# Kernel optimization log

Measured on AMD Instinct MI355X. Metric: run time of the kernel, lower is better.

Reference implementation:

```python
import jax, jax.numpy as jnp
import numpy as np

H, DST, DCONV, EXP = 640, 16, 4, 2
DIN = H * EXP          # 1280
DTR = -(-H // 16)      # 40
EPS = 1e-6


def rmsnorm(x, w):
    rms = jnp.sqrt(jnp.mean(x * x, axis=-1, keepdims=True) + EPS)
    return x / rms * w


def bitlinear(x, w, nw):
    # RMSNorm -> ternary weight quant + int8 activation quant (STE)
    x = rmsnorm(x, nw)
    alpha = jnp.maximum(jnp.mean(jnp.abs(w)), 1e-10)
    wq = jnp.clip(jnp.round(w / alpha), -1.0, 1.0)
    wq = w + jax.lax.stop_gradient(wq - w)
    gamma = jnp.maximum(jnp.max(jnp.abs(x), axis=-1, keepdims=True), 1e-10)
    xq = jnp.clip(jnp.round(x * 127.0 / gamma), -128.0, 127.0)
    xq = x + jax.lax.stop_gradient(xq - x)
    return (xq @ wq.T) * (alpha * gamma / 127.0)


def causal_conv1d(x, cw, cb):
    # x: [B,L,D]; depthwise causal conv, kernel DCONV
    pad = DCONV - 1
    xp = jnp.pad(x, ((0, 0), (pad, 0), (0, 0)))
    L = x.shape[1]
    out = jnp.zeros_like(x)
    for k in range(DCONV):
        out = out + xp[:, pad - k:pad - k + L, :] * cw[:, k]
    return out + cb


def selective_scan(x, dt, B_mat, C_mat, A_log):
    # x,dt: [B,L,D]; B_mat,C_mat: [B,L,N]; A_log: [D,N]
    A = -jnp.exp(A_log)
    dA = jnp.exp(A[None, None] * dt[..., None])                 # [B,L,D,N]
    dBx = dt[..., None] * B_mat[:, :, None, :] * x[..., None]   # [B,L,D,N]
    dA_t = jnp.moveaxis(dA, 1, 0)
    dBx_t = jnp.moveaxis(dBx, 1, 0)
    C_t = jnp.moveaxis(C_mat, 1, 0)

    def step(h, inp):
        da, dbx, c = inp
        h = da * h + dbx
        y = jnp.sum(h * c[:, None, :], axis=-1)  # [B,D]
        return h, y

    h0 = jnp.zeros(x.shape[:1] + (x.shape[2], A_log.shape[1]), x.dtype)
    _, ys = jax.lax.scan(step, h0, (dA_t, dBx_t, C_t))
    return jnp.moveaxis(ys, 0, 1)  # [B,L,D]


def setup_inputs() -> dict:
    key = jax.random.key(0)
    ks = jax.random.split(key, 10)
    sc_in = 1.0 / np.sqrt(H)
    sc_din = 1.0 / np.sqrt(DIN)
    A = np.tile(np.arange(1, DST + 1, dtype=np.float32)[None, :], (DIN, 1))
    return {
        "x": jax.random.normal(ks[0], (2, 2048, H), jnp.float32),
        "norm_w": jnp.ones((H,), jnp.float32),
        "in_w": jax.random.normal(ks[1], (DIN * 2, H), jnp.float32) * sc_in,
        "in_nw": jnp.ones((H,), jnp.float32),
        "conv_w": jax.random.normal(ks[2], (DIN, DCONV), jnp.float32) * 0.1,
        "conv_b": jnp.zeros((DIN,), jnp.float32),
        "dtu_w": jax.random.normal(ks[3], (DTR, DIN), jnp.float32) * sc_din,
        "dtu_nw": jnp.ones((DIN,), jnp.float32),
        "dtd_w": jax.random.normal(ks[4], (DIN, DTR), jnp.float32) / np.sqrt(DTR),
        "dtd_b": jnp.zeros((DIN,), jnp.float32),
        "Bp_w": jax.random.normal(ks[5], (DST, DIN), jnp.float32) * sc_din,
        "Bp_nw": jnp.ones((DIN,), jnp.float32),
        "Cp_w": jax.random.normal(ks[6], (DST, DIN), jnp.float32) * sc_din,
        "Cp_nw": jnp.ones((DIN,), jnp.float32),
        "A_log": jnp.asarray(np.log(A)),
        "D": jnp.ones((DIN,), jnp.float32),
        "out_w": jax.random.normal(ks[7], (H, DIN), jnp.float32) * sc_din,
        "out_nw": jnp.ones((DIN,), jnp.float32),
    }


def reference(x, norm_w, in_w, in_nw, conv_w, conv_b, dtu_w, dtu_nw, dtd_w, dtd_b,
              Bp_w, Bp_nw, Cp_w, Cp_nw, A_log, D, out_w, out_nw):
    residual = x
    xn = rmsnorm(x, norm_w)
    xz = bitlinear(xn, in_w, in_nw)
    x_path, z = jnp.split(xz, 2, axis=-1)
    x_path = causal_conv1d(x_path, conv_w, conv_b)
    x_path = jax.nn.silu(x_path)
    dt = jax.nn.softplus(bitlinear(x_path, dtu_w, dtu_nw) @ dtd_w.T + dtd_b)
    B_mat = bitlinear(x_path, Bp_w, Bp_nw)
    C_mat = bitlinear(x_path, Cp_w, Cp_nw)
    y = selective_scan(x_path, dt, B_mat, C_mat, A_log)
    y = y + x_path * D
    y = y * jax.nn.silu(z)
    return bitlinear(y, out_w, out_nw) + residual
```

## Files before the change

### kernel.cpp

```cpp
#include <hip/hip_runtime.h>
#include <hip/hip_bf16.h>
#include <cmath>

#define NROWS 4096
#define H_    640
#define DIN_  1280
#define DXZ   2560
#define DTR_  40
#define DST_  16
#define LSEQ  2048
#define EPS_  1e-6f
#define NCH   64
#define CL    32
#define NDG   20
#define KSPLIT 8
#define KCH (DIN_ / KSPLIT)
#define LOG2E 1.4426950408889634f
#define RLOG2E 0.6931471805599453f

typedef __attribute__((ext_vector_type(8))) short short8;
typedef __attribute__((ext_vector_type(4))) float f32x4;
typedef unsigned short ushort_t;

__device__ __forceinline__ float bf2f(short u) {
    return __uint_as_float((unsigned)(unsigned short)u << 16);
}
__device__ __forceinline__ short f2bfs(float x) { return (short)(__float_as_uint(x) >> 16); }

#define GLD16(gp, lp) __builtin_amdgcn_global_load_lds( \
    (const __attribute__((address_space(1))) unsigned int*)(unsigned long long)(gp), \
    (__attribute__((address_space(3))) unsigned int*)(unsigned int)(unsigned long long)(lp), 16, 0, 0)

__device__ __forceinline__ float wave_sum64(float v) {
    v += __shfl_xor(v, 1);  v += __shfl_xor(v, 2);  v += __shfl_xor(v, 4);
    v += __shfl_xor(v, 8);  v += __shfl_xor(v, 16); v += __shfl_xor(v, 32);
    return v;
}
__device__ __forceinline__ float wave_max64(float v) {
    v = fmaxf(v, __shfl_xor(v, 1));  v = fmaxf(v, __shfl_xor(v, 2));
    v = fmaxf(v, __shfl_xor(v, 4));  v = fmaxf(v, __shfl_xor(v, 8));
    v = fmaxf(v, __shfl_xor(v, 16)); v = fmaxf(v, __shfl_xor(v, 32));
    return v;
}
__device__ __forceinline__ float block_sum4(float v, float* red4) {
    v = wave_sum64(v);
    if ((threadIdx.x & 63) == 0) red4[threadIdx.x >> 6] = v;
    __syncthreads();
    return (red4[0] + red4[1]) + (red4[2] + red4[3]);
}
__device__ __forceinline__ float block_max4(float v, float* red4) {
    v = wave_max64(v);
    if ((threadIdx.x & 63) == 0) red4[threadIdx.x >> 6] = v;
    __syncthreads();
    return fmaxf(fmaxf(red4[0], red4[1]), fmaxf(red4[2], red4[3]));
}
__device__ __forceinline__ float block_reduce_sum256(float v, float* red) {
    int tid = threadIdx.x;
    red[tid] = v; __syncthreads();
    for (int o = 128; o; o >>= 1) { if (tid < o) red[tid] += red[tid + o]; __syncthreads(); }
    float r = red[0]; __syncthreads();
    return r;
}

__global__ __launch_bounds__(256) void k_pre(const float* __restrict__ x,
                                             const float* __restrict__ norm_w,
                                             const float* __restrict__ in_nw,
                                             const float* __restrict__ w0, const float* __restrict__ w1,
                                             const float* __restrict__ w2, const float* __restrict__ w3,
                                             const float* __restrict__ w4,
                                             int n0, int n1, int n2, int n3, int n4,
                                             __hip_bfloat16* __restrict__ xq, float* __restrict__ gamma,
                                             float* __restrict__ partials) {
    __shared__ float red[256];
    const int tid = threadIdx.x;
    if (blockIdx.x < NROWS) {
        const int r = blockIdx.x;
        const float* xr = x + (size_t)r * H_;
        const bool has2 = (tid < H_ - 512);
        float v0 = xr[tid], v1 = xr[tid + 256], v2 = has2 ? xr[tid + 512] : 0.f;
        float sum = block_sum4(v0 * v0 + v1 * v1 + v2 * v2, red);
        float r1 = 1.f / sqrtf(sum / H_ + EPS_);
        v0 *= r1 * norm_w[tid];
        v1 *= r1 * norm_w[tid + 256];
        if (has2) v2 *= r1 * norm_w[tid + 512];
        sum = block_sum4(v0 * v0 + v1 * v1 + v2 * v2, red + 4);
        float r2 = 1.f / sqrtf(sum / H_ + EPS_);
        v0 *= r2 * in_nw[tid];
        v1 *= r2 * in_nw[tid + 256];
        if (has2) v2 *= r2 * in_nw[tid + 512];
        float mx = fmaxf(fmaxf(fabsf(v0), fabsf(v1)), fabsf(v2));
        float g = fmaxf(block_max4(mx, red + 8), 1e-10f);
        if (tid == 0) gamma[r] = g;
        float s = 127.f / g;
        __hip_bfloat16* o = xq + (size_t)r * H_;
        o[tid]       = __float2bfloat16(fminf(fmaxf(rintf(v0 * s), -128.f), 127.f));
        o[tid + 256] = __float2bfloat16(fminf(fmaxf(rintf(v1 * s), -128.f), 127.f));
        if (has2) o[tid + 512] = __float2bfloat16(fminf(fmaxf(rintf(v2 * s), -128.f), 127.f));
    } else {
        const int flat = blockIdx.x - NROWS;
        const int wi = flat >> 8, xb = flat & 255;
        const float* w = (wi == 0) ? w0 : (wi == 1) ? w1 : (wi == 2) ? w2 : (wi == 3) ? w3 : w4;
        const int n = (wi == 0) ? n0 : (wi == 1) ? n1 : (wi == 2) ? n2 : (wi == 3) ? n3 : n4;
        float s = 0.f;
        for (int i = xb * 256 + tid; i < n; i += 65536) s += fabsf(w[i]);
        float t = block_reduce_sum256(s, red);
        if (tid == 0) partials[wi * 256 + xb] = t;
    }
}

__global__ __launch_bounds__(256) void absmean_final5(const float* __restrict__ partials,
                                                      int n0, int n1, int n2, int n3, int n4,
                                                      float* __restrict__ alphas) {
    const int wi = blockIdx.x;
    const int n = (wi == 0) ? n0 : (wi == 1) ? n1 : (wi == 2) ? n2 : (wi == 3) ? n3 : n4;
    __shared__ double red[256];
    double s = (double)partials[wi * 256 + threadIdx.x];
    red[threadIdx.x] = s; __syncthreads();
    for (int o = 128; o; o >>= 1) { if (threadIdx.x < o) red[threadIdx.x] += red[threadIdx.x + o]; __syncthreads(); }
    if (threadIdx.x == 0) alphas[wi] = fmaxf((float)(red[0] / (double)n), 1e-10f);
}

__global__ __launch_bounds__(256) void k_quant_build(const float* __restrict__ in_w,
                                                     const float* __restrict__ out_w,
                                                     const float* __restrict__ dtu_w,
                                                     const float* __restrict__ Bp_w,
                                                     const float* __restrict__ Cp_w,
                                                     const float* __restrict__ alphas,
                                                     __hip_bfloat16* __restrict__ q_in,
                                                     __hip_bfloat16* __restrict__ q_out,
                                                     ushort_t* __restrict__ wq_sk) {
    const int tid = threadIdx.x;
    if (blockIdx.x < 6400) {
        int i = blockIdx.x * 256 + tid;
        float a = alphas[0];
        ((ushort_t*)q_in)[i] = (ushort_t)f2bfs(fminf(fmaxf(rintf(in_w[i] / a), -1.f), 1.f));
    } else if (blockIdx.x < 9600) {
        int i = (blockIdx.x - 6400) * 256 + tid;
        float a = alphas[4];
        ((ushort_t*)q_out)[i] = (ushort_t)f2bfs(fminf(fmaxf(rintf(out_w[i] / a), -1.f), 1.f));
    } else {
        int idx = (blockIdx.x - 9600) * 256 + tid;
        int t = idx / 2560, rem = idx % 2560, kb = rem / 64, l = rem % 64;
        int nloc = l & 15, kg = l >> 4;
        float alpha; const float* src; int row; bool valid = true;
        if (t < 3)      { alpha = alphas[1]; src = dtu_w; row = t * 16 + nloc; valid = (row < 40); }
        else if (t == 3){ alpha = alphas[2]; src = Bp_w;  row = nloc; }
        else            { alpha = alphas[3]; src = Cp_w;  row = nloc; }
        int k0 = kb * 32 + kg * 8;
        short8 outv;
#pragma unroll
        for (int e = 0; e < 8; ++e) {
            float q = valid ? fminf(fmaxf(rintf(src[(size_t)row * DIN_ + k0 + e] / alpha), -1.f), 1.f) : 0.f;
            outv[e] = f2bfs(q);
        }
        *(short8*)(wq_sk + (size_t)idx * 8) = outv;
    }
}

template<int BM, int BN>
__global__ __launch_bounds__(256) void k_gemm_mfma(const ushort_t* __restrict__ Aq,
                                                   const ushort_t* __restrict__ Wq,
                                                   const float* __restrict__ alpha_p,
                                                   const float* __restrict__ gamma,
                                                   const float* __restrict__ residual,
                                                   float* __restrict__ out,
                                                   int M, int N, int K) {
    constexpr int FM = BM / 32, FN = BN / 32;
    constexpr int NL = (BM + BN) / 64;
    __shared__ ushort_t As[2][BM * 32];
    __shared__ ushort_t Bs[2][BN * 32];
    const int tid = threadIdx.x;
    const int w = tid >> 6, lane = tid & 63;
    const int wm = w >> 1, wn = w & 1;
    const int nwg = gridDim.x * gridDim.y;
    const int hw = blockIdx.y * gridDim.x + blockIdx.x;
    const int work = (nwg % 8 == 0) ? ((hw & 7) * (nwg >> 3) + (hw >> 3)) : hw;
    const int row0 = (work / gridDim.x) * BM;
    const int col0 = (work % gridDim.x) * BN;
    f32x4 acc[FM][FN] = {};

    auto stage = [&](int buf, int k0) {
        #pragma unroll
        for (int q = 0; q < BM / 64; ++q) {
            int c = w * BM + q * 64 + lane;
            int row = c >> 2;
            int uslot = (c & 3) ^ (row & 3);
            GLD16(Aq + (size_t)(row0 + row) * K + k0 + uslot * 8,
                  (char*)As[buf] + (w * BM + q * 64) * 16);
        }
        #pragma unroll
        for (int q = 0; q < BN / 64; ++q) {
            int c = w * BN + q * 64 + lane;
            int row = c >> 2;
            int uslot = (c & 3) ^ (row & 3);
            GLD16(Wq + (size_t)(col0 + row) * K + k0 + uslot * 8,
                  (char*)Bs[buf] + (w * BN + q * 64) * 16);
        }
    };

    stage(0, 0);
    const int NT = K >> 5;
    for (int t = 0; t < NT; ++t) {
        const int cur = t & 1;
        if (t + 1 < NT) {
            stage(cur ^ 1, (t + 1) << 5);
            if constexpr (NL == 2)      asm volatile("s_waitcnt vmcnt(2)" ::: "memory");
            else if constexpr (NL == 3) asm volatile("s_waitcnt vmcnt(3)" ::: "memory");
            else                        asm volatile("s_waitcnt vmcnt(4)" ::: "memory");
        } else {
            asm volatile("s_waitcnt vmcnt(0)" ::: "memory");
        }
        __builtin_amdgcn_s_barrier();

        short8 a[FM], b[FN];
        #pragma unroll
        for (int i = 0; i < FM; ++i) {
            int row = wm * (BM / 2) + i * 16 + (lane & 15);
            int byt = row * 64 + (((lane >> 4) ^ (row & 3)) << 4);
            a[i] = *(const short8*)((const char*)As[cur] + byt);
        }
        #pragma unroll
        for (int j = 0; j < FN; ++j) {
            int row = wn * (BN / 2) + j * 16 + (lane & 15);
            int byt = row * 64 + (((lane >> 4) ^ (row & 3)) << 4);
            b[j] = *(const short8*)((const char*)Bs[cur] + byt);
        }
        #pragma unroll
        for (int i = 0; i < FM; ++i)
            #pragma unroll
            for (int j = 0; j < FN; ++j)
                acc[i][j] = __builtin_amdgcn_mfma_f32_16x16x32_bf16(a[i], b[j], acc[i][j], 0, 0, 0);
        asm volatile("" ::: "memory");
        __builtin_amdgcn_s_barrier();
    }

    const float alpha = alpha_p[0];
    #pragma unroll
    for (int i = 0; i < FM; ++i) {
        #pragma unroll
        for (int r = 0; r < 4; ++r) {
            int row = row0 + wm * (BM / 2) + i * 16 + (lane >> 4) * 4 + r;
            float s = alpha * gamma[row] * (1.f / 127.f);
            #pragma unroll
            for (int j = 0; j < FN; ++j) {
                int col = col0 + wn * (BN / 2) + j * 16 + (lane & 15);
                float o = acc[i][j][r] * s;
                if (residual) o += residual[(size_t)row * N + col];
                out[(size_t)row * N + col] = o;
            }
        }
    }
}

__global__ __launch_bounds__(256) void k_conv_norm(const float* __restrict__ xz,
                                                   const float* __restrict__ cw, const float* __restrict__ cb,
                                                   const float* __restrict__ dtu_nw,
                                                   const float* __restrict__ Bp_nw,
                                                   const float* __restrict__ Cp_nw,
                                                   float* __restrict__ xp,
                                                   float* __restrict__ rinv_out, float* __restrict__ g3) {
    const int row = blockIdx.x, tid = threadIdx.x;
    const int l = row & (LSEQ - 1);
    __shared__ float red4[16];
    float vv[5];
    float ss = 0.f;
#pragma unroll
    for (int j = 0; j < 5; ++j) {
        int d = tid + j * 256;
        f32x4 c4 = *(const f32x4*)(cw + (size_t)d * 4);
        const float* base = xz + (size_t)row * DXZ + d;
        float s = cb[d] + base[0] * c4[0];
        if (l >= 1) s += base[-(ptrdiff_t)DXZ] * c4[1];
        if (l >= 2) s += base[-(ptrdiff_t)(2 * DXZ)] * c4[2];
        if (l >= 3) s += base[-(ptrdiff_t)(3 * DXZ)] * c4[3];
        float v = s / (1.f + __builtin_amdgcn_exp2f(-s * LOG2E));
        vv[j] = v;
        ss += v * v;
        xp[(size_t)row * DIN_ + d] = v;
    }
    float sum = block_sum4(ss, red4);
    float rms = 1.f / sqrtf(sum / DIN_ + EPS_);
    float m0 = 0.f, m1 = 0.f, m2 = 0.f;
#pragma unroll
    for (int j = 0; j < 5; ++j) {
        int d = tid + j * 256;
        float t = vv[j] * rms;
        m0 = fmaxf(m0, fabsf(t * dtu_nw[d]));
        m1 = fmaxf(m1, fabsf(t * Bp_nw[d]));
        m2 = fmaxf(m2, fabsf(t * Cp_nw[d]));
    }
    float g0 = block_max4(m0, red4 + 4);
    float g1 = block_max4(m1, red4 + 8);
    float g2 = block_max4(m2, red4 + 12);
    if (tid == 0) {
        rinv_out[row]       = rms;
        g3[row]             = fmaxf(g0, 1e-10f);
        g3[NROWS + row]     = fmaxf(g1, 1e-10f);
        g3[2 * NROWS + row] = fmaxf(g2, 1e-10f);
    }
}

__global__ __launch_bounds__(256) void k_skinny_mfma(const float* __restrict__ xp,
                                                     const float* __restrict__ rinv,
                                                     const float* __restrict__ dtu_nw,
                                                     const float* __restrict__ Bp_nw,
                                                     const float* __restrict__ Cp_nw,
                                                     const float* __restrict__ g3,
                                                     const ushort_t* __restrict__ wq_sk,
                                                     float* __restrict__ dtu_acc,
                                                     float* __restrict__ B_acc,
                                                     float* __restrict__ C_acc) {
    const int tid = threadIdx.x;
    const int w = tid >> 6, l = tid & 63;
    const int row0 = blockIdx.x * 64;
    const int kc0 = blockIdx.y * KCH;
    __shared__ float s_xp[64 * 36];
    __shared__ float s_nw[3 * KCH];
    for (int i = tid; i < 3 * KCH; i += 256) {
        int m = i / KCH, j = i - m * KCH;
        const float* nw = (m == 0) ? dtu_nw : (m == 1) ? Bp_nw : Cp_nw;
        s_nw[i] = nw[kc0 + j];
    }
    const int arow = row0 + w * 16 + (l & 15);
    const float ri = rinv[arow];
    const float s0 = 127.f / g3[arow];
    const float s1 = 127.f / g3[NROWS + arow];
    const float s2 = 127.f / g3[2 * NROWS + arow];
    const int kgrp = l >> 4;
    f32x4 acc[5] = {};

    for (int ks = 0; ks < KCH / 32; ++ks) {
        const int kc = kc0 + ks * 32;
        __syncthreads();
        {
            int srow = tid >> 2, scol = (tid & 3) * 8;
            const float* gp = xp + (size_t)(row0 + srow) * DIN_ + kc + scol;
            f32x4 u0 = *(const f32x4*)gp;
            f32x4 u1 = *(const f32x4*)(gp + 4);
            *(f32x4*)(s_xp + srow * 36 + scol)     = u0;
            *(f32x4*)(s_xp + srow * 36 + scol + 4) = u1;
        }
        __syncthreads();
        const float* sp = s_xp + (w * 16 + (l & 15)) * 36 + kgrp * 8;
        f32x4 t0 = *(const f32x4*)sp;
        f32x4 t1 = *(const f32x4*)(sp + 4);
        float t[8] = { t0[0]*ri, t0[1]*ri, t0[2]*ri, t0[3]*ri,
                       t1[0]*ri, t1[1]*ri, t1[2]*ri, t1[3]*ri };
        short8 a0, a1, a2;
        #pragma unroll
        for (int e = 0; e < 8; ++e) {
            int kk = ks * 32 + kgrp * 8 + e;
            float q0 = fminf(fmaxf(rintf(t[e] * s_nw[kk]           * s0), -128.f), 127.f);
            float q1 = fminf(fmaxf(rintf(t[e] * s_nw[KCH + kk]     * s1), -128.f), 127.f);
            float q2 = fminf(fmaxf(rintf(t[e] * s_nw[2 * KCH + kk] * s2), -128.f), 127.f);
            a0[e] = f2bfs(q0); a1[e] = f2bfs(q1); a2[e] = f2bfs(q2);
        }
        const int kbg = kc >> 5;
        short8 b0 = *(const short8*)(wq_sk + ((size_t)(0 * 40 + kbg) * 64 + l) * 8);
        short8 b1 = *(const short8*)(wq_sk + ((size_t)(1 * 40 + kbg) * 64 + l) * 8);
        short8 b2 = *(const short8*)(wq_sk + ((size_t)(2 * 40 + kbg) * 64 + l) * 8);
        short8 b3 = *(const short8*)(wq_sk + ((size_t)(3 * 40 + kbg) * 64 + l) * 8);
        short8 b4 = *(const short8*)(wq_sk + ((size_t)(4 * 40 + kbg) * 64 + l) * 8);
        acc[0] = __builtin_amdgcn_mfma_f32_16x16x32_bf16(a0, b0, acc[0], 0, 0, 0);
        acc[1] = __builtin_amdgcn_mfma_f32_16x16x32_bf16(a0, b1, acc[1], 0, 0, 0);
        acc[2] = __builtin_amdgcn_mfma_f32_16x16x32_bf16(a0, b2, acc[2], 0, 0, 0);
        acc[3] = __builtin_amdgcn_mfma_f32_16x16x32_bf16(a1, b3, acc[3], 0, 0, 0);
        acc[4] = __builtin_amdgcn_mfma_f32_16x16x32_bf16(a2, b4, acc[4], 0, 0, 0);
    }

    const int col = l & 15;
    const int rbase = row0 + w * 16 + (l >> 4) * 4;
    #pragma unroll
    for (int j = 0; j < 4; ++j) {
        int r = rbase + j;
        atomicAdd(&dtu_acc[(size_t)r * DTR_ + col],      acc[0][j]);
        atomicAdd(&dtu_acc[(size_t)r * DTR_ + 16 + col], acc[1][j]);
        if (col < 8) atomicAdd(&dtu_acc[(size_t)r * DTR_ + 32 + col], acc[2][j]);
        atomicAdd(&B_acc[(size_t)r * DST_ + col], acc[3][j]);
        atomicAdd(&C_acc[(size_t)r * DST_ + col], acc[4][j]);
    }
}

__global__ __launch_bounds__(256) void k_dtd(const float* __restrict__ U,
                                             const float* __restrict__ W,
                                             const float* __restrict__ bias,
                                             const float* __restrict__ g3,
                                             const float* __restrict__ alphas,
                                             float* __restrict__ dt) {
    const int c0 = blockIdx.x * 64;
    const int r0 = blockIdx.y * 32;
    const int tid = threadIdx.x;
    const int col = tid & 63, rg = tid >> 6;
    __shared__ float s_w[64 * 41];
    __shared__ float s_u[32 * 40];
    for (int i = tid; i < 64 * 40; i += 256) {
        int cc = i / 40, t = i - cc * 40;
        s_w[cc * 41 + t] = W[(size_t)c0 * 40 + i];
    }
    const float alpha = alphas[1];
    for (int i = tid; i < 32 * 40; i += 256) {
        int rr = i / 40;
        s_u[i] = ((U[(size_t)r0 * 40 + i] * alpha) * g3[r0 + rr]) * (1.f / 127.f);
    }
    __syncthreads();
    float w[40];
#pragma unroll
    for (int t = 0; t < 40; t++) w[t] = s_w[col * 41 + t];
    const float b = bias[c0 + col];
    for (int r8 = 0; r8 < 8; ++r8) {
        const int row = rg * 8 + r8;
        const float* ur = s_u + row * 40;
        float a0 = b, a1 = 0.f, a2 = 0.f, a3 = 0.f;
#pragma unroll
        for (int t = 0; t < 40; t += 4) {
            f32x4 uv = *(const f32x4*)(ur + t);
            a0 = fmaf(uv[0], w[t],     a0);
            a1 = fmaf(uv[1], w[t + 1], a1);
            a2 = fmaf(uv[2], w[t + 2], a2);
            a3 = fmaf(uv[3], w[t + 3], a3);
        }
        float s = (a0 + a1) + (a2 + a3);
        float e = __builtin_amdgcn_exp2f(-fabsf(s) * LOG2E);
        float sp = fmaxf(s, 0.f) + __builtin_amdgcn_logf(1.f + e) * RLOG2E;
        dt[(size_t)(r0 + row) * DIN_ + c0 + col] = sp;
    }
}

__global__ __launch_bounds__(256) void k_scan_a(const float* __restrict__ dt, const float* __restrict__ xp,
                                                const float* __restrict__ Bm, const float* __restrict__ A_log,
                                                const float* __restrict__ g3, const float* __restrict__ alphas,
                                                float* __restrict__ hloc, float* __restrict__ sdt_out) {
    const int tid = threadIdx.x;
    const int q = tid & 3, dloc = tid >> 2;
    const int dg = blockIdx.x, c = blockIdx.y, b = blockIdx.z;
    const int d = dg * 64 + dloc;
    const int l0 = c * CL;
    __shared__ float s_B[CL * 16];
    if (tid < CL * 4) {
        int rg = b * LSEQ + l0 + (tid >> 2);
        float a2 = alphas[2];
        float gB = g3[NROWS + rg];
        f32x4 Bv = *(const f32x4*)(Bm + (size_t)rg * DST_ + (tid & 3) * 4);
        f32x4 o;
#pragma unroll
        for (int k = 0; k < 4; ++k) o[k] = ((Bv[k] * a2) * gB) * (1.f / 127.f);
        *(f32x4*)(s_B + tid * 4) = o;
    }
    f32x4 Av = *(const f32x4*)(A_log + (size_t)d * DST_ + q * 4);
    float A2[4];
#pragma unroll
    for (int j = 0; j < 4; ++j) A2[j] = -expf(Av[j]) * LOG2E;
    __syncthreads();
    const float* dtp = dt + (size_t)(b * LSEQ + l0) * DIN_ + d;
    const float* xpp = xp + (size_t)(b * LSEQ + l0) * DIN_ + d;
    float h[4] = {};
    float sdt = 0.f;
    float dtv = *dtp, xv = *xpp;
    for (int l = 0; l < CL; ++l) {
        float ndt = 0.f, nx = 0.f;
        if (l + 1 < CL) { ndt = dtp[(size_t)(l + 1) * DIN_]; nx = xpp[(size_t)(l + 1) * DIN_]; }
        f32x4 Bv = *(const f32x4*)(s_B + l * 16 + q * 4);
        float dtx = dtv * xv;
        sdt += dtv;
#pragma unroll
        for (int j = 0; j < 4; ++j) {
            float dA = __builtin_amdgcn_exp2f(A2[j] * dtv);
            h[j] = fmaf(dA, h[j], Bv[j] * dtx);
        }
        dtv = ndt; xv = nx;
    }
    size_t base = ((size_t)(b * NDG + dg) * 64 + c) * 1024 + tid * 4;
    *(f32x4*)(hloc + base) = (f32x4){h[0], h[1], h[2], h[3]};
    if (q == 0) sdt_out[((size_t)(b * NDG + dg) * 64 + c) * 64 + dloc] = sdt;
}

__global__ __launch_bounds__(256) void k_scan_b(float* __restrict__ hloc, const float* __restrict__ sdt,
                                                const float* __restrict__ A_log) {
    const int tid = threadIdx.x;
    const int idx = blockIdx.x;
    const int b = idx / (NDG * 64);
    const int rem = idx % (NDG * 64);
    const int dg = rem / 64, dloc = rem % 64;
    const int d = dg * 64 + dloc;
    __shared__ float s_h[64 * 17];
    __shared__ float s_sdt[64];
    __shared__ float s_A2[16];
    const size_t gb = (size_t)(b * NDG + dg) * 64;
#pragma unroll
    for (int i = 0; i < 4; ++i) {
        int c = i * 16 + (tid >> 4), n = tid & 15;
        s_h[c * 17 + n] = hloc[(gb + c) * 1024 + dloc * 16 + n];
    }
    if (tid < 64) s_sdt[tid] = sdt[(gb + tid) * 64 + dloc];
    else if (tid < 80) s_A2[tid - 64] = -expf(A_log[(size_t)d * DST_ + (tid - 64)]) * LOG2E;
    __syncthreads();
    const int w = tid >> 6, lane = tid & 63;
#pragma unroll
    for (int nn = 0; nn < 4; ++nn) {
        int n = w * 4 + nn;
        float h = s_h[lane * 17 + n];
        float P = __builtin_amdgcn_exp2f(s_A2[n] * s_sdt[lane]);
#pragma unroll
        for (int s = 1; s < 64; s <<= 1) {
            float hp = __shfl_up(h, s);
            float Pp = __shfl_up(P, s);
            if (lane >= s) { h = fmaf(P, hp, h); P *= Pp; }
        }
        float Hi = __shfl_up(h, 1);
        if (lane == 0) Hi = 0.f;
        s_h[lane * 17 + n] = Hi;
    }
    __syncthreads();
#pragma unroll
    for (int i = 0; i < 4; ++i) {
        int c = i * 16 + (tid >> 4), n = tid & 15;
        hloc[(gb + c) * 1024 + dloc * 16 + n] = s_h[c * 17 + n];
    }
}

__global__ __launch_bounds__(256) void k_scan_c(const float* __restrict__ dt, const float* __restrict__ xp,
                                                const float* __restrict__ Bm, const float* __restrict__ Cm,
                                                const float* __restrict__ xz, const float* __restrict__ A_log,
                                                const float* __restrict__ Dvec, const float* __restrict__ g3,
                                                const float* __restrict__ alphas,
                                                const float* __restrict__ Hinit, float* __restrict__ y) {
    const int tid = threadIdx.x;
    const int q = tid & 3, dloc = tid >> 2;
    const int dg = blockIdx.x, c = blockIdx.y, b = blockIdx.z;
    const int d = dg * 64 + dloc;
    const int l0 = c * CL;
    __shared__ float s_B[CL * 16], s_C[CL * 16];
    if (tid < CL * 4) {
        int rg = b * LSEQ + l0 + (tid >> 2);
        float a2 = alphas[2];
        float gB = g3[NROWS + rg];
        f32x4 Bv = *(const f32x4*)(Bm + (size_t)rg * DST_ + (tid & 3) * 4);
        f32x4 o;
#pragma unroll
        for (int k = 0; k < 4; ++k) o[k] = ((Bv[k] * a2) * gB) * (1.f / 127.f);
        *(f32x4*)(s_B + tid * 4) = o;
    } else {
        int t2 = tid - CL * 4;
        int rg = b * LSEQ + l0 + (t2 >> 2);
        float a3 = alphas[3];
        float gC = g3[2 * NROWS + rg];
        f32x4 Cv = *(const f32x4*)(Cm + (size_t)rg * DST_ + (t2 & 3) * 4);
        f32x4 o;
#pragma unroll
        for (int k = 0; k < 4; ++k) o[k] = ((Cv[k] * a3) * gC) * (1.f / 127.f);
        *(f32x4*)(s_C + t2 * 4) = o;
    }
    f32x4 Av = *(const f32x4*)(A_log + (size_t)d * DST_ + q * 4);
    float A2[4];
#pragma unroll
    for (int j = 0; j < 4; ++j) A2[j] = -expf(Av[j]) * LOG2E;
    const float Dd = Dvec[d];
    __syncthreads();
    const float* dtp = dt + (size_t)(b * LSEQ + l0) * DIN_ + d;
    const float* xpp = xp + (size_t)(b * LSEQ + l0) * DIN_ + d;
    const float* zp  = xz + (size_t)(b * LSEQ + l0) * DXZ + DIN_ + d;
    float* yp = y + (size_t)(b * LSEQ + l0) * DIN_ + d;
    size_t base = ((size_t)(b * NDG + dg) * 64 + c) * 1024 + tid * 4;
    f32x4 hv = *(const f32x4*)(Hinit + base);
    float h[4] = {hv[0], hv[1], hv[2], hv[3]};
    float dtv = *dtp, xv = *xpp, zv = *zp;
    for (int l = 0; l < CL; ++l) {
        float ndt = 0.f, nx = 0.f, nz = 0.f;
        if (l + 1 < CL) {
            ndt = dtp[(size_t)(l + 1) * DIN_];
            nx  = xpp[(size_t)(l + 1) * DIN_];
            nz  = zp[(size_t)(l + 1) * DXZ];
        }
        f32x4 Bv = *(const f32x4*)(s_B + l * 16 + q * 4);
        f32x4 Cv = *(const f32x4*)(s_C + l * 16 + q * 4);
        float dtx = dtv * xv;
        float yv = 0.f;
#pragma unroll
        for (int j = 0; j < 4; ++j) {
            float dA = __builtin_amdgcn_exp2f(A2[j] * dtv);
            h[j] = fmaf(dA, h[j], Bv[j] * dtx);
            yv = fmaf(h[j], Cv[j], yv);
        }
        yv += __shfl_xor(yv, 1);
        yv += __shfl_xor(yv, 2);
        if (q == 0) {
            float sig = 1.f / (1.f + __builtin_amdgcn_exp2f(-zv * LOG2E));
            yp[(size_t)l * DIN_] = (yv + xv * Dd) * (zv * sig);
        }
        dtv = ndt; xv = nx; zv = nz;
    }
}

__global__ __launch_bounds__(256) void k_norm_y(const float* __restrict__ y,
                                                const float* __restrict__ out_nw,
                                                __hip_bfloat16* __restrict__ yq, float* __restrict__ gy) {
    const int r = blockIdx.x, tid = threadIdx.x;
    const float* yr = y + (size_t)r * DIN_;
    __shared__ float red4[8];
    float v[5];
    float ss = 0.f;
#pragma unroll
    for (int j = 0; j < 5; j++) { v[j] = yr[tid + j * 256]; ss += v[j] * v[j]; }
    float sum = block_sum4(ss, red4);
    float rms = 1.f / sqrtf(sum / DIN_ + EPS_);
    float mx = 0.f;
#pragma unroll
    for (int j = 0; j < 5; j++) {
        int i = tid + j * 256;
        v[j] = v[j] * rms * out_nw[i];
        mx = fmaxf(mx, fabsf(v[j]));
    }
    float g = fmaxf(block_max4(mx, red4 + 4), 1e-10f);
    if (tid == 0) gy[r] = g;
    float s = 127.f / g;
#pragma unroll
    for (int j = 0; j < 5; j++) {
        int i = tid + j * 256;
        yq[(size_t)r * DIN_ + i] = __float2bfloat16(fminf(fmaxf(rintf(v[j] * s), -128.f), 127.f));
    }
}

extern "C" void kernel_launch(void* const* d_in, const int* in_sizes, int n_in,
                              void* d_out, int out_size, void* d_ws, size_t ws_size,
                              hipStream_t stream) {
    (void)in_sizes; (void)n_in; (void)out_size;
    const float* x      = (const float*)d_in[0];
    const float* norm_w = (const float*)d_in[1];
    const float* in_w   = (const float*)d_in[2];
    const float* in_nw  = (const float*)d_in[3];
    const float* conv_w = (const float*)d_in[4];
    const float* conv_b = (const float*)d_in[5];
    const float* dtu_w  = (const float*)d_in[6];
    const float* dtu_nw = (const float*)d_in[7];
    const float* dtd_w  = (const float*)d_in[8];
    const float* dtd_b  = (const float*)d_in[9];
    const float* Bp_w   = (const float*)d_in[10];
    const float* Bp_nw  = (const float*)d_in[11];
    const float* Cp_w   = (const float*)d_in[12];
    const float* Cp_nw  = (const float*)d_in[13];
    const float* A_log  = (const float*)d_in[14];
    const float* Dv     = (const float*)d_in[15];
    const float* out_w  = (const float*)d_in[16];
    const float* out_nw = (const float*)d_in[17];

    float* ws = (float*)d_ws;
    float* alphas   = ws;
    float* partials = ws + 8;
    float* xq1      = ws + 8 + 5 * 256;
    float* gamma1   = xq1 + (size_t)NROWS * H_;
    float* xz       = gamma1 + NROWS;
    float* xp       = xz + (size_t)NROWS * DXZ;
    float* xpn     = xp + (size_t)NROWS * DIN_;
    float* g3       = xpn + (size_t)NROWS * DIN_;
    float* dtu_out  = g3 + 3 * NROWS;
    float* Bmat     = dtu_out + (size_t)NROWS * DTR_;
    float* Cmat     = Bmat + (size_t)NROWS * DST_;
    float* dtb      = Cmat + (size_t)NROWS * DST_;
    float* gy       = dtb + (size_t)NROWS * DIN_;
    float* wq_in    = gy + NROWS;
    float* wq_dtu   = wq_in + (size_t)DXZ * H_;
    float* wq_Bp    = wq_dtu + (size_t)DTR_ * DIN_;
    float* wq_Cp    = wq_Bp + (size_t)DST_ * DIN_;
    float* wq_out   = wq_Cp + (size_t)DST_ * DIN_;
    float* rinv     = wq_out + (size_t)H_ * DIN_;
    float* wq_sk    = rinv + NROWS;
    float* sdt      = wq_sk + 51200;
    size_t need = (size_t)((sdt + 2 * NDG * 64 * 64) - ws) * sizeof(float);
    if (ws_size < need) return;

    float* hloc = xq1;

    hipMemsetAsync(dtu_out, 0, (size_t)NROWS * 72 * sizeof(float), stream);

    const int n0 = DXZ * H_, n1 = DTR_ * DIN_, n2 = DST_ * DIN_, n3 = DST_ * DIN_, n4 = H_ * DIN_;
    hipLaunchKernelGGL(k_pre, dim3(NROWS + 5 * 256), dim3(256), 0, stream,
                       x, norm_w, in_nw, in_w, dtu_w, Bp_w, Cp_w, out_w,
                       n0, n1, n2, n3, n4, (__hip_bfloat16*)xq1, gamma1, partials);
    hipLaunchKernelGGL(absmean_final5, dim3(5), dim3(256), 0, stream, partials, n0, n1, n2, n3, n4, alphas);
    hipLaunchKernelGGL(k_quant_build, dim3(9650), dim3(256), 0, stream,
                       in_w, out_w, dtu_w, Bp_w, Cp_w, alphas,
                       (__hip_bfloat16*)wq_in, (__hip_bfloat16*)wq_out, (ushort_t*)wq_sk);

    hipLaunchKernelGGL((k_gemm_mfma<128, 128>), dim3(DXZ / 128, NROWS / 128), dim3(256), 0, stream,
                       (const ushort_t*)xq1, (const ushort_t*)wq_in, alphas + 0, gamma1,
                       (const float*)nullptr, xz, NROWS, DXZ, H_);
    hipLaunchKernelGGL(k_conv_norm, dim3(NROWS), dim3(256), 0, stream,
                       xz, conv_w, conv_b, dtu_nw, Bp_nw, Cp_nw, xp, rinv, g3);
    hipLaunchKernelGGL(k_skinny_mfma, dim3(NROWS / 64, KSPLIT), dim3(256), 0, stream,
                       xp, rinv, dtu_nw, Bp_nw, Cp_nw, g3, (const ushort_t*)wq_sk,
                       dtu_out, Bmat, Cmat);
    hipLaunchKernelGGL(k_dtd, dim3(DIN_ / 64, NROWS / 32), dim3(256), 0, stream,
                       dtu_out, dtd_w, dtd_b, g3, alphas, dtb);

    hipLaunchKernelGGL(k_scan_a, dim3(NDG, NCH, 2), dim3(256), 0, stream,
                       dtb, xp, Bmat, A_log, g3, alphas, hloc, sdt);
    hipLaunchKernelGGL(k_scan_b, dim3(2 * NDG * 64), dim3(256), 0, stream, hloc, sdt, A_log);
    hipLaunchKernelGGL(k_scan_c, dim3(NDG, NCH, 2), dim3(256), 0, stream,
                       dtb, xp, Bmat, Cmat, xz, A_log, Dv, g3, alphas, hloc, xpn );

    hipLaunchKernelGGL(k_norm_y, dim3(NROWS), dim3(256), 0, stream, xpn , out_nw,
                       (__hip_bfloat16*)dtb , gy);
    hipLaunchKernelGGL((k_gemm_mfma<64, 64>), dim3(H_ / 64, NROWS / 64), dim3(256), 0, stream,
                       (const ushort_t*)dtb , (const ushort_t*)wq_out, alphas + 4, gy,
                       x , (float*)d_out, NROWS, H_, DIN_);
}
```

Baseline: 227.5 us.

## Fuse dt projection and softplus into scan kernels, drop standalone dt kernel

Removes the separate k_dtd kernel. Each scan block (scan_a and scan_c) now recomputes its 32x64 dt tile from the low-rank dtu output and dtd weights in shared memory, then reads dt from LDS instead of global memory. This removes a kernel launch and the write plus two reads of the 4096x1280 dt tensor. In exchange the dt arithmetic runs twice and each block uses more shared memory. The input GEMM tile is also changed from 128x128 to 128x64.

```diff
diff --git a/kernel.cpp b/kernel.cpp
--- a/kernel.cpp
+++ b/kernel.cpp
@@ -381,52 +381,36 @@
     }
 }
 
-__global__ __launch_bounds__(256) void k_dtd(const float* __restrict__ U,
-                                             const float* __restrict__ W,
-                                             const float* __restrict__ bias,
-                                             const float* __restrict__ g3,
-                                             const float* __restrict__ alphas,
-                                             float* __restrict__ dt) {
-    const int c0 = blockIdx.x * 64;
-    const int r0 = blockIdx.y * 32;
-    const int tid = threadIdx.x;
-    const int col = tid & 63, rg = tid >> 6;
-    __shared__ float s_w[64 * 41];
-    __shared__ float s_u[32 * 40];
-    for (int i = tid; i < 64 * 40; i += 256) {
-        int cc = i / 40, t = i - cc * 40;
-        s_w[cc * 41 + t] = W[(size_t)c0 * 40 + i];
-    }
-    const float alpha = alphas[1];
-    for (int i = tid; i < 32 * 40; i += 256) {
-        int rr = i / 40;
-        s_u[i] = ((U[(size_t)r0 * 40 + i] * alpha) * g3[r0 + rr]) * (1.f / 127.f);
-    }
-    __syncthreads();
-    float w[40];
-#pragma unroll
-    for (int t = 0; t < 40; t++) w[t] = s_w[col * 41 + t];
-    const float b = bias[c0 + col];
-    for (int r8 = 0; r8 < 8; ++r8) {
-        const int row = rg * 8 + r8;
-        const float* ur = s_u + row * 40;
-        float a0 = b, a1 = 0.f, a2 = 0.f, a3 = 0.f;
+__device__ __forceinline__ void compute_dt_tile(const float* __restrict__ s_u,
+                                                const float* __restrict__ s_w,
+                                                float* __restrict__ s_dt,
+                                                int q, int dloc, float bd) {
+    float wreg[40];
+#pragma unroll
+    for (int t = 0; t < 40; ++t) wreg[t] = s_w[dloc * 41 + t];
+#pragma unroll
+    for (int j = 0; j < 8; ++j) {
+        const int l = q * 8 + j;
+        const float* ur = s_u + l * 40;
+        float a0 = bd, a1 = 0.f, a2 = 0.f, a3 = 0.f;
 #pragma unroll
         for (int t = 0; t < 40; t += 4) {
             f32x4 uv = *(const f32x4*)(ur + t);
-            a0 = fmaf(uv[0], w[t],     a0);
-            a1 = fmaf(uv[1], w[t + 1], a1);
-            a2 = fmaf(uv[2], w[t + 2], a2);
-            a3 = fmaf(uv[3], w[t + 3], a3);
+            a0 = fmaf(uv[0], wreg[t],     a0);
+            a1 = fmaf(uv[1], wreg[t + 1], a1);
+            a2 = fmaf(uv[2], wreg[t + 2], a2);
+            a3 = fmaf(uv[3], wreg[t + 3], a3);
         }
         float s = (a0 + a1) + (a2 + a3);
         float e = __builtin_amdgcn_exp2f(-fabsf(s) * LOG2E);
-        float sp = fmaxf(s, 0.f) + __builtin_amdgcn_logf(1.f + e) * RLOG2E;
-        dt[(size_t)(r0 + row) * DIN_ + c0 + col] = sp;
-    }
-}
-
-__global__ __launch_bounds__(256) void k_scan_a(const float* __restrict__ dt, const float* __restrict__ xp,
+        s_dt[dloc * 33 + l] = fmaxf(s, 0.f) + __builtin_amdgcn_logf(1.f + e) * RLOG2E;
+    }
+}
+
+__global__ __launch_bounds__(256) void k_scan_a(const float* __restrict__ U ,
+                                                const float* __restrict__ dtd_w,
+                                                const float* __restrict__ dtd_b,
+                                                const float* __restrict__ xp,
                                                 const float* __restrict__ Bm, const float* __restrict__ A_log,
                                                 const float* __restrict__ g3, const float* __restrict__ alphas,
                                                 float* __restrict__ hloc, float* __restrict__ sdt_out) {
@@ -435,9 +419,13 @@
     const int dg = blockIdx.x, c = blockIdx.y, b = blockIdx.z;
     const int d = dg * 64 + dloc;
     const int l0 = c * CL;
+    const int r0 = b * LSEQ + l0;
     __shared__ float s_B[CL * 16];
+    __shared__ float s_u[32 * 40];
+    __shared__ float s_w[64 * 41];
+    __shared__ float s_dt[64 * 33];
     if (tid < CL * 4) {
-        int rg = b * LSEQ + l0 + (tid >> 2);
+        int rg = r0 + (tid >> 2);
         float a2 = alphas[2];
         float gB = g3[NROWS + rg];
         f32x4 Bv = *(const f32x4*)(Bm + (size_t)rg * DST_ + (tid & 3) * 4);
@@ -446,19 +434,33 @@
         for (int k = 0; k < 4; ++k) o[k] = ((Bv[k] * a2) * gB) * (1.f / 127.f);
         *(f32x4*)(s_B + tid * 4) = o;
     }
+    {
+        const float alpha1 = alphas[1];
+        for (int i = tid; i < 32 * 40; i += 256) {
+            int rr = i / 40;
+            s_u[i] = ((U[(size_t)r0 * 40 + i] * alpha1) * g3[r0 + rr]) * (1.f / 127.f);
+        }
+        for (int i = tid; i < 64 * 40; i += 256) {
+            int cc = i / 40, t = i - cc * 40;
+            s_w[cc * 41 + t] = dtd_w[(size_t)(dg * 64) * 40 + i];
+        }
+    }
     f32x4 Av = *(const f32x4*)(A_log + (size_t)d * DST_ + q * 4);
     float A2[4];
 #pragma unroll
     for (int j = 0; j < 4; ++j) A2[j] = -expf(Av[j]) * LOG2E;
+    const float bd = dtd_b[d];
     __syncthreads();
-    const float* dtp = dt + (size_t)(b * LSEQ + l0) * DIN_ + d;
-    const float* xpp = xp + (size_t)(b * LSEQ + l0) * DIN_ + d;
+    compute_dt_tile(s_u, s_w, s_dt, q, dloc, bd);
+    __syncthreads();
+
+    const float* xpp = xp + (size_t)r0 * DIN_ + d;
     float h[4] = {};
     float sdt = 0.f;
-    float dtv = *dtp, xv = *xpp;
+    float xv = *xpp;
     for (int l = 0; l < CL; ++l) {
-        float ndt = 0.f, nx = 0.f;
-        if (l + 1 < CL) { ndt = dtp[(size_t)(l + 1) * DIN_]; nx = xpp[(size_t)(l + 1) * DIN_]; }
+        float nx = (l + 1 < CL) ? xpp[(size_t)(l + 1) * DIN_] : 0.f;
+        float dtv = s_dt[dloc * 33 + l];
         f32x4 Bv = *(const f32x4*)(s_B + l * 16 + q * 4);
         float dtx = dtv * xv;
         sdt += dtv;
@@ -467,7 +469,7 @@
             float dA = __builtin_amdgcn_exp2f(A2[j] * dtv);
             h[j] = fmaf(dA, h[j], Bv[j] * dtx);
         }
-        dtv = ndt; xv = nx;
+        xv = nx;
     }
     size_t base = ((size_t)(b * NDG + dg) * 64 + c) * 1024 + tid * 4;
     *(f32x4*)(hloc + base) = (f32x4){h[0], h[1], h[2], h[3]};
@@ -518,7 +520,10 @@
     }
 }
 
-__global__ __launch_bounds__(256) void k_scan_c(const float* __restrict__ dt, const float* __restrict__ xp,
+__global__ __launch_bounds__(256) void k_scan_c(const float* __restrict__ U,
+                                                const float* __restrict__ dtd_w,
+                                                const float* __restrict__ dtd_b,
+                                                const float* __restrict__ xp,
                                                 const float* __restrict__ Bm, const float* __restrict__ Cm,
                                                 const float* __restrict__ xz, const float* __restrict__ A_log,
                                                 const float* __restrict__ Dvec, const float* __restrict__ g3,
@@ -529,9 +534,13 @@
     const int dg = blockIdx.x, c = blockIdx.y, b = blockIdx.z;
     const int d = dg * 64 + dloc;
     const int l0 = c * CL;
+    const int r0 = b * LSEQ + l0;
     __shared__ float s_B[CL * 16], s_C[CL * 16];
+    __shared__ float s_u[32 * 40];
+    __shared__ float s_w[64 * 41];
+    __shared__ float s_dt[64 * 33];
     if (tid < CL * 4) {
-        int rg = b * LSEQ + l0 + (tid >> 2);
+        int rg = r0 + (tid >> 2);
         float a2 = alphas[2];
         float gB = g3[NROWS + rg];
         f32x4 Bv = *(const f32x4*)(Bm + (size_t)rg * DST_ + (tid & 3) * 4);
@@ -541,7 +550,7 @@
         *(f32x4*)(s_B + tid * 4) = o;
     } else {
         int t2 = tid - CL * 4;
-        int rg = b * LSEQ + l0 + (t2 >> 2);
+        int rg = r0 + (t2 >> 2);
         float a3 = alphas[3];
         float gC = g3[2 * NROWS + rg];
         f32x4 Cv = *(const f32x4*)(Cm + (size_t)rg * DST_ + (t2 & 3) * 4);
@@ -550,27 +559,41 @@
         for (int k = 0; k < 4; ++k) o[k] = ((Cv[k] * a3) * gC) * (1.f / 127.f);
         *(f32x4*)(s_C + t2 * 4) = o;
     }
+    {
+        const float alpha1 = alphas[1];
+        for (int i = tid; i < 32 * 40; i += 256) {
+            int rr = i / 40;
+            s_u[i] = ((U[(size_t)r0 * 40 + i] * alpha1) * g3[r0 + rr]) * (1.f / 127.f);
+        }
+        for (int i = tid; i < 64 * 40; i += 256) {
+            int cc = i / 40, t = i - cc * 40;
+            s_w[cc * 41 + t] = dtd_w[(size_t)(dg * 64) * 40 + i];
+        }
+    }
     f32x4 Av = *(const f32x4*)(A_log + (size_t)d * DST_ + q * 4);
     float A2[4];
 #pragma unroll
     for (int j = 0; j < 4; ++j) A2[j] = -expf(Av[j]) * LOG2E;
     const float Dd = Dvec[d];
+    const float bd = dtd_b[d];
     __syncthreads();
-    const float* dtp = dt + (size_t)(b * LSEQ + l0) * DIN_ + d;
-    const float* xpp = xp + (size_t)(b * LSEQ + l0) * DIN_ + d;
-    const float* zp  = xz + (size_t)(b * LSEQ + l0) * DXZ + DIN_ + d;
-    float* yp = y + (size_t)(b * LSEQ + l0) * DIN_ + d;
+    compute_dt_tile(s_u, s_w, s_dt, q, dloc, bd);
+    __syncthreads();
+
+    const float* xpp = xp + (size_t)r0 * DIN_ + d;
+    const float* zp  = xz + (size_t)r0 * DXZ + DIN_ + d;
+    float* yp = y + (size_t)r0 * DIN_ + d;
     size_t base = ((size_t)(b * NDG + dg) * 64 + c) * 1024 + tid * 4;
     f32x4 hv = *(const f32x4*)(Hinit + base);
     float h[4] = {hv[0], hv[1], hv[2], hv[3]};
-    float dtv = *dtp, xv = *xpp, zv = *zp;
+    float xv = *xpp, zv = *zp;
     for (int l = 0; l < CL; ++l) {
-        float ndt = 0.f, nx = 0.f, nz = 0.f;
+        float nx = 0.f, nz = 0.f;
         if (l + 1 < CL) {
-            ndt = dtp[(size_t)(l + 1) * DIN_];
-            nx  = xpp[(size_t)(l + 1) * DIN_];
-            nz  = zp[(size_t)(l + 1) * DXZ];
-        }
+            nx = xpp[(size_t)(l + 1) * DIN_];
+            nz = zp[(size_t)(l + 1) * DXZ];
+        }
+        float dtv = s_dt[dloc * 33 + l];
         f32x4 Bv = *(const f32x4*)(s_B + l * 16 + q * 4);
         f32x4 Cv = *(const f32x4*)(s_C + l * 16 + q * 4);
         float dtx = dtv * xv;
@@ -587,7 +610,7 @@
             float sig = 1.f / (1.f + __builtin_amdgcn_exp2f(-zv * LOG2E));
             yp[(size_t)l * DIN_] = (yv + xv * Dd) * (zv * sig);
         }
-        dtv = ndt; xv = nx; zv = nz;
+        xv = nx; zv = nz;
     }
 }
 
@@ -681,7 +704,7 @@
                        in_w, out_w, dtu_w, Bp_w, Cp_w, alphas,
                        (__hip_bfloat16*)wq_in, (__hip_bfloat16*)wq_out, (ushort_t*)wq_sk);
 
-    hipLaunchKernelGGL((k_gemm_mfma<128, 128>), dim3(DXZ / 128, NROWS / 128), dim3(256), 0, stream,
+    hipLaunchKernelGGL((k_gemm_mfma<128, 64>), dim3(DXZ / 64, NROWS / 128), dim3(256), 0, stream,
                        (const ushort_t*)xq1, (const ushort_t*)wq_in, alphas + 0, gamma1,
                        (const float*)nullptr, xz, NROWS, DXZ, H_);
     hipLaunchKernelGGL(k_conv_norm, dim3(NROWS), dim3(256), 0, stream,
@@ -689,14 +712,13 @@
     hipLaunchKernelGGL(k_skinny_mfma, dim3(NROWS / 64, KSPLIT), dim3(256), 0, stream,
                        xp, rinv, dtu_nw, Bp_nw, Cp_nw, g3, (const ushort_t*)wq_sk,
                        dtu_out, Bmat, Cmat);
-    hipLaunchKernelGGL(k_dtd, dim3(DIN_ / 64, NROWS / 32), dim3(256), 0, stream,
-                       dtu_out, dtd_w, dtd_b, g3, alphas, dtb);
 
     hipLaunchKernelGGL(k_scan_a, dim3(NDG, NCH, 2), dim3(256), 0, stream,
-                       dtb, xp, Bmat, A_log, g3, alphas, hloc, sdt);
+                       dtu_out, dtd_w, dtd_b, xp, Bmat, A_log, g3, alphas, hloc, sdt);
     hipLaunchKernelGGL(k_scan_b, dim3(2 * NDG * 64), dim3(256), 0, stream, hloc, sdt, A_log);
     hipLaunchKernelGGL(k_scan_c, dim3(NDG, NCH, 2), dim3(256), 0, stream,
-                       dtb, xp, Bmat, Cmat, xz, A_log, Dv, g3, alphas, hloc, xpn );
+                       dtu_out, dtd_w, dtd_b, xp, Bmat, Cmat, xz, A_log, Dv, g3, alphas,
+                       hloc, xpn );
 
     hipLaunchKernelGGL(k_norm_y, dim3(NROWS), dim3(256), 0, stream, xpn , out_nw,
                        (__hip_bfloat16*)dtb , gy);
```

Result: slower. 269.3 us (+18.4%).
